# Optimization experiments

Measured on AMD Instinct MI355X. Metric: run time of the kernel, lower is better.

## Reference

```python
import jax, jax.numpy as jnp
import numpy as np

N = 8192
IN_F = 256
OUT_F = 256
ATTN_DIM = 2
NEG_INF = -1e18


def setup_inputs() -> dict:
    key = jax.random.key(0)
    k1, k2, k3, k4, k5 = jax.random.split(key, 5)
    node_feats = jax.random.normal(k1, (N, IN_F), dtype=jnp.float32)
    Ahat = (jax.random.uniform(k2, (N, N)) < 0.01).astype(jnp.float32)
    # ensure no isolated rows (self loops) so softmax rows are well-defined
    Ahat = Ahat.at[jnp.arange(N), jnp.arange(N)].set(1.0)
    bound_w = 1.0 / np.sqrt(IN_F)
    bound_wa = 1.0 / np.sqrt(OUT_F)
    bound_a = 1.0 / np.sqrt(2 * ATTN_DIM)
    w = jax.random.uniform(k3, (IN_F, OUT_F), minval=-bound_w, maxval=bound_w, dtype=jnp.float32)
    w_a = jax.random.uniform(k4, (OUT_F, ATTN_DIM), minval=-bound_wa, maxval=bound_wa, dtype=jnp.float32)
    a = jax.random.uniform(k5, (2 * ATTN_DIM, 1), minval=-bound_a, maxval=bound_a, dtype=jnp.float32)
    return {"node_feats": node_feats, "Ahat": Ahat, "w": w, "w_a": w_a, "a": a}


def reference(node_feats, Ahat, w, w_a, a):
    # h_prime: [N, out_features]
    h_prime = node_feats @ w
    # h_reduced: [N, attn_dim]
    h_reduced = h_prime @ w_a
    # e[i, j] = cat(h_red[i], h_red[j]) @ a  ==  h_red[i]@a[:d] + h_red[j]@a[d:]
    # (identical math to the repeat+cat+matmul in the original, without the
    #  O(N^2 * 2d) materialization)
    f_src = (h_reduced @ a[:ATTN_DIM]).squeeze(-1)  # [N]
    f_dst = (h_reduced @ a[ATTN_DIM:]).squeeze(-1)  # [N]
    e = f_src[:, None] + f_dst[None, :]             # [N, N]
    masked_e = jnp.where(Ahat > 0, e, NEG_INF)
    attn_scores = jax.nn.softmax(masked_e, axis=-1)  # [N, N]
    out = attn_scores @ h_prime                      # [N, out_features]
    return jax.nn.relu(out)
```

## Files before the change

kernel.cpp:

```cpp
#include <hip/hip_runtime.h>
#include <hip/hip_bf16.h>
#include <math.h>

#define NN 8192
#define IN_F 256
#define OUT_F 256

typedef _Float16 half4_t __attribute__((ext_vector_type(4)));
typedef float    f4_t    __attribute__((ext_vector_type(4)));

#define KC 32
#define LS 68
#define CAPW 192
#define GEMM_BLOCKS 512
#define SCAN_BLOCKS 2048

__global__ __launch_bounds__(256) void scan_and_gemm(
    const float* __restrict__ Ahat,
    const float* __restrict__ X,
    const float* __restrict__ W,
    _Float16* __restrict__ H16,
    int* __restrict__ g_idx,
    int* __restrict__ g_cnt)
{
    __shared__ float smem[2 * KC * LS];
    const int bid = blockIdx.x;
    const int tid = threadIdx.x;

    if (bid < GEMM_BLOCKS) {
        float* As = smem;
        float* Bs = smem + KC * LS;
        const int row0 = (bid & 127) * 64;
        const int col0 = (bid >> 7) * 64;
        const int tx = tid & 15;
        const int ty = tid >> 4;

        float acc[4][4];
#pragma unroll
        for (int i = 0; i < 4; ++i)
#pragma unroll
            for (int j = 0; j < 4; ++j) acc[i][j] = 0.0f;

        for (int k0 = 0; k0 < IN_F; k0 += KC) {
            {
                const int k4 = tid & 7;
                const int r0 = tid >> 3;
#pragma unroll
                for (int rp = 0; rp < 2; ++rp) {
                    const int r = r0 + rp * 32;
                    const float4 v = *(const float4*)(X + (size_t)(row0 + r) * IN_F + k0 + k4 * 4);
                    As[(k4 * 4 + 0) * LS + r] = v.x;
                    As[(k4 * 4 + 1) * LS + r] = v.y;
                    As[(k4 * 4 + 2) * LS + r] = v.z;
                    As[(k4 * 4 + 3) * LS + r] = v.w;
                }
            }
            {
                const int c4 = tid & 15;
                const int kb = tid >> 4;
#pragma unroll
                for (int kp = 0; kp < 2; ++kp) {
                    const int k = kb + kp * 16;
                    *(float4*)(&Bs[k * LS + c4 * 4]) =
                        *(const float4*)(W + (size_t)(k0 + k) * OUT_F + col0 + c4 * 4);
                }
            }
            __syncthreads();

#pragma unroll
            for (int k = 0; k < KC; ++k) {
                const float4 av = *(const float4*)(&As[k * LS + ty * 4]);
                const float4 bv = *(const float4*)(&Bs[k * LS + tx * 4]);
                const float a_[4] = {av.x, av.y, av.z, av.w};
                const float b_[4] = {bv.x, bv.y, bv.z, bv.w};
#pragma unroll
                for (int i = 0; i < 4; ++i)
#pragma unroll
                    for (int j = 0; j < 4; ++j)
                        acc[i][j] = fmaf(a_[i], b_[j], acc[i][j]);
            }
            __syncthreads();
        }

#pragma unroll
        for (int i = 0; i < 4; ++i) {
            half4_t o;
            o.x = (_Float16)acc[i][0];
            o.y = (_Float16)acc[i][1];
            o.z = (_Float16)acc[i][2];
            o.w = (_Float16)acc[i][3];
            *(half4_t*)(H16 + (size_t)(row0 + ty * 4 + i) * OUT_F + col0 + tx * 4) = o;
        }
        return;
    }

    int* s_idx = (int*)smem;
    const int wid  = tid >> 6;
    const int lane = tid & 63;
    const int row  = (bid - GEMM_BLOCKS) * 4 + wid;
    int* const my_idx = s_idx + wid * CAPW;

    const f4_t* arow = (const f4_t*)(Ahat + (size_t)row * NN);

    int cnt = 0;
    f4_t cur[4], nxt[4];
#pragma unroll
    for (int q = 0; q < 4; ++q)
        cur[q] = __builtin_nontemporal_load(arow + q * 64 + lane);

#pragma unroll
    for (int g = 0; g < 8; ++g) {
        if (g < 7) {
#pragma unroll
            for (int q = 0; q < 4; ++q)
                nxt[q] = __builtin_nontemporal_load(arow + ((g + 1) * 4 + q) * 64 + lane);
        }

#pragma unroll
        for (int q = 0; q < 4; ++q) {
            const f4_t v = cur[q];
            const int jbase = (g * 4 + q) * 256 + lane * 4;

#define COMPACT(pred, comp)                                                   \
            {                                                                 \
                const unsigned long long m = __ballot(pred);                  \
                const unsigned int lo =                                       \
                    __builtin_amdgcn_mbcnt_lo((unsigned)m, 0);                \
                const int pos = cnt + (int)__builtin_amdgcn_mbcnt_hi(         \
                                            (unsigned)(m >> 32), lo);         \
                if ((pred) && pos < CAPW) my_idx[pos] = jbase + (comp);       \
                cnt += __builtin_popcountll(m);                               \
            }

            COMPACT(v.x > 0.0f, 0)
            COMPACT(v.y > 0.0f, 1)
            COMPACT(v.z > 0.0f, 2)
            COMPACT(v.w > 0.0f, 3)
#undef COMPACT
        }

#pragma unroll
        for (int q = 0; q < 4; ++q) cur[q] = nxt[q];
    }
    if (cnt > CAPW) cnt = CAPW;

    for (int k = lane; k < cnt; k += 64)
        g_idx[(size_t)row * CAPW + k] = my_idx[k];
    if (lane == 0) g_cnt[row] = cnt;
}

__global__ __launch_bounds__(256) void fdst_exp(
    const _Float16* __restrict__ hp16,
    const float* __restrict__ w_a,
    const float* __restrict__ a,
    float* __restrict__ fexp)
{
    const int row  = blockIdx.x * 4 + (threadIdx.x >> 6);
    const int lane = threadIdx.x & 63;

    const float a2 = a[2];
    const float a3 = a[3];

    const half4_t h  = ((const half4_t*)hp16)[(size_t)row * 64 + lane];
    const float4 wa0 = *(const float4*)(w_a + lane * 8);
    const float4 wa1 = *(const float4*)(w_a + lane * 8 + 4);

    float s = (float)h.x * fmaf(wa0.x, a2, wa0.y * a3)
            + (float)h.y * fmaf(wa0.z, a2, wa0.w * a3)
            + (float)h.z * fmaf(wa1.x, a2, wa1.y * a3)
            + (float)h.w * fmaf(wa1.z, a2, wa1.w * a3);

#pragma unroll
    for (int off = 32; off > 0; off >>= 1) s += __shfl_xor(s, off, 64);

    if (lane == 0) fexp[row] = expf(s);
}

__global__ __launch_bounds__(256) void gather_aggregate(
    const _Float16* __restrict__ hp16,
    const float* __restrict__ fexp,
    const int* __restrict__ g_idx,
    const int* __restrict__ g_cnt,
    float* __restrict__ out)
{
    const int wid  = threadIdx.x >> 6;
    const int lane = threadIdx.x & 63;
    const int row  = blockIdx.x * 4 + wid;

    const int cnt = g_cnt[row];
    const int* idx = g_idx + (size_t)row * CAPW;
    const half4_t* hp4 = (const half4_t*)hp16;

    float4 acc = {0.0f, 0.0f, 0.0f, 0.0f};
    float den = 0.0f;

    int k = 0;
    for (; k + 8 <= cnt; k += 8) {
        const int4 ja = *(const int4*)(idx + k);
        const int4 jb = *(const int4*)(idx + k + 4);

        const float p0 = fexp[ja.x], p1 = fexp[ja.y], p2 = fexp[ja.z], p3 = fexp[ja.w];
        const float p4 = fexp[jb.x], p5 = fexp[jb.y], p6 = fexp[jb.z], p7 = fexp[jb.w];

        const half4_t h0 = hp4[((size_t)ja.x << 6) + lane];
        const half4_t h1 = hp4[((size_t)ja.y << 6) + lane];
        const half4_t h2 = hp4[((size_t)ja.z << 6) + lane];
        const half4_t h3 = hp4[((size_t)ja.w << 6) + lane];
        const half4_t h4 = hp4[((size_t)jb.x << 6) + lane];
        const half4_t h5 = hp4[((size_t)jb.y << 6) + lane];
        const half4_t h6 = hp4[((size_t)jb.z << 6) + lane];
        const half4_t h7 = hp4[((size_t)jb.w << 6) + lane];

        acc.x = fmaf(p0, (float)h0.x, acc.x); acc.y = fmaf(p0, (float)h0.y, acc.y);
        acc.z = fmaf(p0, (float)h0.z, acc.z); acc.w = fmaf(p0, (float)h0.w, acc.w);
        acc.x = fmaf(p1, (float)h1.x, acc.x); acc.y = fmaf(p1, (float)h1.y, acc.y);
        acc.z = fmaf(p1, (float)h1.z, acc.z); acc.w = fmaf(p1, (float)h1.w, acc.w);
        acc.x = fmaf(p2, (float)h2.x, acc.x); acc.y = fmaf(p2, (float)h2.y, acc.y);
        acc.z = fmaf(p2, (float)h2.z, acc.z); acc.w = fmaf(p2, (float)h2.w, acc.w);
        acc.x = fmaf(p3, (float)h3.x, acc.x); acc.y = fmaf(p3, (float)h3.y, acc.y);
        acc.z = fmaf(p3, (float)h3.z, acc.z); acc.w = fmaf(p3, (float)h3.w, acc.w);
        acc.x = fmaf(p4, (float)h4.x, acc.x); acc.y = fmaf(p4, (float)h4.y, acc.y);
        acc.z = fmaf(p4, (float)h4.z, acc.z); acc.w = fmaf(p4, (float)h4.w, acc.w);
        acc.x = fmaf(p5, (float)h5.x, acc.x); acc.y = fmaf(p5, (float)h5.y, acc.y);
        acc.z = fmaf(p5, (float)h5.z, acc.z); acc.w = fmaf(p5, (float)h5.w, acc.w);
        acc.x = fmaf(p6, (float)h6.x, acc.x); acc.y = fmaf(p6, (float)h6.y, acc.y);
        acc.z = fmaf(p6, (float)h6.z, acc.z); acc.w = fmaf(p6, (float)h6.w, acc.w);
        acc.x = fmaf(p7, (float)h7.x, acc.x); acc.y = fmaf(p7, (float)h7.y, acc.y);
        acc.z = fmaf(p7, (float)h7.z, acc.z); acc.w = fmaf(p7, (float)h7.w, acc.w);

        den += ((p0 + p1) + (p2 + p3)) + ((p4 + p5) + (p6 + p7));
    }
    for (; k < cnt; ++k) {
        const int j = idx[k];
        const float p = fexp[j];
        const half4_t h = hp4[((size_t)j << 6) + lane];
        acc.x = fmaf(p, (float)h.x, acc.x);
        acc.y = fmaf(p, (float)h.y, acc.y);
        acc.z = fmaf(p, (float)h.z, acc.z);
        acc.w = fmaf(p, (float)h.w, acc.w);
        den += p;
    }

    const float inv = 1.0f / den;
    float4 o;
    o.x = fmaxf(acc.x * inv, 0.0f);
    o.y = fmaxf(acc.y * inv, 0.0f);
    o.z = fmaxf(acc.z * inv, 0.0f);
    o.w = fmaxf(acc.w * inv, 0.0f);
    *(float4*)(out + (size_t)row * OUT_F + lane * 4) = o;
}

extern "C" void kernel_launch(void* const* d_in, const int* in_sizes, int n_in,
                              void* d_out, int out_size, void* d_ws, size_t ws_size,
                              hipStream_t stream) {
    const float* node_feats = (const float*)d_in[0];
    const float* Ahat       = (const float*)d_in[1];
    const float* w          = (const float*)d_in[2];
    const float* w_a        = (const float*)d_in[3];
    const float* a          = (const float*)d_in[4];
    float* out = (float*)d_out;

    char* ws = (char*)d_ws;
    _Float16* hp16 = (_Float16*)ws;
    float* fexp    = (float*)(ws + 4194304);
    int* g_cnt     = (int*)(ws + 4194304 + 32768);
    int* g_idx     = (int*)(ws + 4194304 + 65536);

    scan_and_gemm<<<dim3(GEMM_BLOCKS + SCAN_BLOCKS), 256, 0, stream>>>(
        Ahat, node_feats, w, hp16, g_idx, g_cnt);

    fdst_exp<<<dim3(NN / 4), 256, 0, stream>>>(hp16, w_a, a, fexp);

    gather_aggregate<<<dim3(NN / 4), 256, 0, stream>>>(hp16, fexp, g_idx, g_cnt, out);
}
```

Before: 397.6 us.

## Replace per-row index compaction with grid-stride bitmask sweep and in-gather decoding

The adjacency scan no longer compacts column indices per row with serial ballot/prefix logic. It now sweeps Ahat in a flat grid-stride pattern and writes only 64-bit ballot bitmasks (1 bit per entry) to workspace. The gather kernel decodes each row's bitmask with a wave prefix sum and writes the indices into shared memory before aggregating. This aims to make the bandwidth-bound 256MB scan a simpler, more uniformly streaming loop with fewer dependent instructions per chunk. The cost is extra decode work and shared-memory index construction in the gather kernel.

```diff
diff --git a/kernel.cpp b/kernel.cpp
--- a/kernel.cpp
+++ b/kernel.cpp
@@ -8,20 +8,22 @@
 
 typedef _Float16 half4_t __attribute__((ext_vector_type(4)));
 typedef float    f4_t    __attribute__((ext_vector_type(4)));
+typedef unsigned long long u64;
+typedef u64 u64x2 __attribute__((ext_vector_type(2)));
 
 #define KC 32
 #define LS 68
 #define CAPW 192
 #define GEMM_BLOCKS 512
-#define SCAN_BLOCKS 2048
-
-__global__ __launch_bounds__(256) void scan_and_gemm(
+#define SWEEP_BLOCKS 1536
+#define TOTAL_CHUNKS (NN * NN / 256)
+
+__global__ __launch_bounds__(256) void sweep_and_gemm(
     const float* __restrict__ Ahat,
     const float* __restrict__ X,
     const float* __restrict__ W,
     _Float16* __restrict__ H16,
-    int* __restrict__ g_idx,
-    int* __restrict__ g_cnt)
+    u64* __restrict__ bm)
 {
     __shared__ float smem[2 * KC * LS];
     const int bid = blockIdx.x;
@@ -94,59 +96,37 @@
         return;
     }
 
-    int* s_idx = (int*)smem;
+    const int sb   = bid - GEMM_BLOCKS;
     const int wid  = tid >> 6;
     const int lane = tid & 63;
-    const int row  = (bid - GEMM_BLOCKS) * 4 + wid;
-    int* const my_idx = s_idx + wid * CAPW;
-
-    const f4_t* arow = (const f4_t*)(Ahat + (size_t)row * NN);
-
-    int cnt = 0;
-    f4_t cur[4], nxt[4];
-#pragma unroll
-    for (int q = 0; q < 4; ++q)
-        cur[q] = __builtin_nontemporal_load(arow + q * 64 + lane);
-
-#pragma unroll
-    for (int g = 0; g < 8; ++g) {
-        if (g < 7) {
-#pragma unroll
-            for (int q = 0; q < 4; ++q)
-                nxt[q] = __builtin_nontemporal_load(arow + ((g + 1) * 4 + q) * 64 + lane);
-        }
-
-#pragma unroll
-        for (int q = 0; q < 4; ++q) {
-            const f4_t v = cur[q];
-            const int jbase = (g * 4 + q) * 256 + lane * 4;
-
-#define COMPACT(pred, comp)                                                   \
-            {                                                                 \
-                const unsigned long long m = __ballot(pred);                  \
-                const unsigned int lo =                                       \
-                    __builtin_amdgcn_mbcnt_lo((unsigned)m, 0);                \
-                const int pos = cnt + (int)__builtin_amdgcn_mbcnt_hi(         \
-                                            (unsigned)(m >> 32), lo);         \
-                if ((pred) && pos < CAPW) my_idx[pos] = jbase + (comp);       \
-                cnt += __builtin_popcountll(m);                               \
-            }
-
-            COMPACT(v.x > 0.0f, 0)
-            COMPACT(v.y > 0.0f, 1)
-            COMPACT(v.z > 0.0f, 2)
-            COMPACT(v.w > 0.0f, 3)
-#undef COMPACT
-        }
-
-#pragma unroll
-        for (int q = 0; q < 4; ++q) cur[q] = nxt[q];
-    }
-    if (cnt > CAPW) cnt = CAPW;
-
-    for (int k = lane; k < cnt; k += 64)
-        g_idx[(size_t)row * CAPW + k] = my_idx[k];
-    if (lane == 0) g_cnt[row] = cnt;
+    const f4_t* af4 = (const f4_t*)Ahat;
+
+#define PROCESS_CHUNK(vv, cc)                                                 \
+    {                                                                         \
+        const u64 m0 = __ballot((vv).x > 0.0f);                               \
+        const u64 m1 = __ballot((vv).y > 0.0f);                               \
+        const u64 m2 = __ballot((vv).z > 0.0f);                               \
+        const u64 m3 = __ballot((vv).w > 0.0f);                               \
+        if (lane < 4) {                                                       \
+            const u64 mv = (lane == 0) ? m0 : (lane == 1) ? m1                \
+                          : (lane == 2) ? m2 : m3;                            \
+            bm[((size_t)((cc) >> 5) << 7) + (((cc) & 31) << 2) + lane] = mv;  \
+        }                                                                     \
+    }
+
+    int c = sb * 4 + wid;
+    f4_t v = __builtin_nontemporal_load(af4 + (size_t)c * 64 + lane);
+    for (int it = 0; it < 42; ++it) {
+        const int cn = c + SWEEP_BLOCKS * 4;
+        f4_t vn;
+        if (cn < TOTAL_CHUNKS)
+            vn = __builtin_nontemporal_load(af4 + (size_t)cn * 64 + lane);
+        PROCESS_CHUNK(v, c)
+        v = vn;
+        c = cn;
+    }
+    if (c < TOTAL_CHUNKS) PROCESS_CHUNK(v, c)
+#undef PROCESS_CHUNK
 }
 
 __global__ __launch_bounds__(256) void fdst_exp(
@@ -177,27 +157,60 @@
 }
 
 __global__ __launch_bounds__(256) void gather_aggregate(
+    const u64* __restrict__ bm,
     const _Float16* __restrict__ hp16,
     const float* __restrict__ fexp,
-    const int* __restrict__ g_idx,
-    const int* __restrict__ g_cnt,
     float* __restrict__ out)
 {
+    __shared__ int s_idx[4 * CAPW];
+
     const int wid  = threadIdx.x >> 6;
     const int lane = threadIdx.x & 63;
     const int row  = blockIdx.x * 4 + wid;
-
-    const int cnt = g_cnt[row];
-    const int* idx = g_idx + (size_t)row * CAPW;
+    int* const my_idx = s_idx + wid * CAPW;
+
+    const u64x2 w2 = *(const u64x2*)(bm + ((size_t)row << 7) + (lane << 1));
+    const int myCnt = __builtin_popcountll(w2.x) + __builtin_popcountll(w2.y);
+
+    int pre = myCnt;
+#pragma unroll
+    for (int off = 1; off < 64; off <<= 1) {
+        const int n = __shfl_up(pre, off, 64);
+        if (lane >= off) pre += n;
+    }
+    const int total = __shfl(pre, 63, 64);
+    int pos = pre - myCnt;
+
+    {
+        const int W0 = lane << 1;
+        const int base0 = ((W0 >> 2) << 8) + (W0 & 3);
+        u64 m = w2.x;
+        while (m) {
+            const int b = __builtin_ctzll(m);
+            m &= m - 1;
+            if (pos < CAPW) my_idx[pos] = base0 + (b << 2);
+            ++pos;
+        }
+        const int W1 = W0 + 1;
+        const int base1 = ((W1 >> 2) << 8) + (W1 & 3);
+        m = w2.y;
+        while (m) {
+            const int b = __builtin_ctzll(m);
+            m &= m - 1;
+            if (pos < CAPW) my_idx[pos] = base1 + (b << 2);
+            ++pos;
+        }
+    }
+    const int cnt = (total < CAPW) ? total : CAPW;
+
     const half4_t* hp4 = (const half4_t*)hp16;
-
     float4 acc = {0.0f, 0.0f, 0.0f, 0.0f};
     float den = 0.0f;
 
     int k = 0;
     for (; k + 8 <= cnt; k += 8) {
-        const int4 ja = *(const int4*)(idx + k);
-        const int4 jb = *(const int4*)(idx + k + 4);
+        const int4 ja = *(const int4*)(my_idx + k);
+        const int4 jb = *(const int4*)(my_idx + k + 4);
 
         const float p0 = fexp[ja.x], p1 = fexp[ja.y], p2 = fexp[ja.z], p3 = fexp[ja.w];
         const float p4 = fexp[jb.x], p5 = fexp[jb.y], p6 = fexp[jb.z], p7 = fexp[jb.w];
@@ -231,7 +244,7 @@
         den += ((p0 + p1) + (p2 + p3)) + ((p4 + p5) + (p6 + p7));
     }
     for (; k < cnt; ++k) {
-        const int j = idx[k];
+        const int j = my_idx[k];
         const float p = fexp[j];
         const half4_t h = hp4[((size_t)j << 6) + lane];
         acc.x = fmaf(p, (float)h.x, acc.x);
@@ -263,13 +276,12 @@
     char* ws = (char*)d_ws;
     _Float16* hp16 = (_Float16*)ws;
     float* fexp    = (float*)(ws + 4194304);
-    int* g_cnt     = (int*)(ws + 4194304 + 32768);
-    int* g_idx     = (int*)(ws + 4194304 + 65536);
-
-    scan_and_gemm<<<dim3(GEMM_BLOCKS + SCAN_BLOCKS), 256, 0, stream>>>(
-        Ahat, node_feats, w, hp16, g_idx, g_cnt);
+    u64* bm        = (u64*)(ws + 4227072);
+
+    sweep_and_gemm<<<dim3(GEMM_BLOCKS + SWEEP_BLOCKS), 256, 0, stream>>>(
+        Ahat, node_feats, w, hp16, bm);
 
     fdst_exp<<<dim3(NN / 4), 256, 0, stream>>>(hp16, w_a, a, fexp);
 
-    gather_aggregate<<<dim3(NN / 4), 256, 0, stream>>>(hp16, fexp, g_idx, g_cnt, out);
-}
+    gather_aggregate<<<dim3(NN / 4), 256, 0, stream>>>(bm, hp16, fexp, out);
+}
```

Measured after the change: 394.2 us. About the same (-0.9%).
